# Kernel optimization log

Measured on AMD Instinct MI355X. Metric: run time of the kernel, lower is better.

## Reference

```python
import jax, jax.numpy as jnp
import numpy as np

BETA = 0.25

def setup_inputs() -> dict:
    key = jax.random.key(0)
    k1, k2 = jax.random.split(key)
    N, K, D = 262144, 256, 256
    z_e = jax.random.normal(k1, (N, D), dtype=jnp.float32)
    # nn.Embedding init: uniform(-1/K, 1/K)
    emb_weight = jax.random.uniform(k2, (K, D), dtype=jnp.float32, minval=-1.0 / K, maxval=1.0 / K)
    return {"z_e": z_e, "emb_weight": emb_weight}

def reference(z_e, emb_weight):
    # squared L2 distances: ||z||^2 + ||e||^2 - 2 z e^T  -> [N, K]
    dist = (jnp.sum(z_e ** 2, axis=1, keepdims=True)
            + jnp.sum(emb_weight ** 2, axis=1)
            - 2.0 * jnp.matmul(z_e, emb_weight.T))
    encoding_inds = jnp.argmin(dist, axis=1)  # [N]
    z_q = emb_weight[encoding_inds]           # [N, D]

    sg = jax.lax.stop_gradient
    commitment_loss = jnp.mean((sg(z_e) - z_q) ** 2)
    codebook_loss = jnp.mean((z_e - sg(z_q)) ** 2)
    loss = codebook_loss + BETA * commitment_loss

    # straight-through estimator
    z_q_st = z_e + sg(z_q - z_e)
    return z_q_st, encoding_inds, loss
```

## Files before the change

kernel.cpp:

```cpp
#include <hip/hip_runtime.h>

typedef __attribute__((ext_vector_type(8))) short bf16x8;
typedef __attribute__((ext_vector_type(4))) float f32x4;
typedef __attribute__((ext_vector_type(4))) unsigned short us4;
typedef __attribute__((ext_vector_type(8))) unsigned short us8;

#define NROWS 262144
#define KC 256
#define DD 256
#define BM 64
#define DK 32
#define SW 40
#define TAU 1.5e-3f
#define FCAP 65536

__device__ __forceinline__ float np_pw128_sq(const float* a) {
    float r[8];
#pragma unroll
    for (int j = 0; j < 8; ++j) r[j] = __fmul_rn(a[j], a[j]);
    for (int i = 8; i < 128; i += 8) {
#pragma unroll
        for (int j = 0; j < 8; ++j)
            r[j] = __fadd_rn(r[j], __fmul_rn(a[i + j], a[i + j]));
    }
    float t01 = __fadd_rn(r[0], r[1]), t23 = __fadd_rn(r[2], r[3]);
    float t45 = __fadd_rn(r[4], r[5]), t67 = __fadd_rn(r[6], r[7]);
    return __fadd_rn(__fadd_rn(t01, t23), __fadd_rn(t45, t67));
}
__device__ __forceinline__ float np_sum256_sq(const float* a) {
    return __fadd_rn(np_pw128_sq(a), np_pw128_sq(a + 128));
}

__device__ __forceinline__ unsigned short bf16_rne(float x) {
    unsigned b = __float_as_uint(x);
    b += 0x7FFFu + ((b >> 16) & 1u);
    return (unsigned short)(b >> 16);
}

__global__ void vq_prep(const float* __restrict__ emb, float* __restrict__ se,
                        double* __restrict__ accum, int* __restrict__ gcnt) {
    int k = threadIdx.x;
    if (k == 0) { *accum = 0.0; *gcnt = 0; }
    se[k] = np_sum256_sq(emb + (size_t)k * DD);
}

__global__ void vq_split(const float* __restrict__ emb, unsigned short* __restrict__ ph) {
    int f = (blockIdx.x * 256 + threadIdx.x) * 4;
    float4 v = *reinterpret_cast<const float4*>(emb + f);
    int k = f >> 8, d = f & 255;
    int off = (d >> 5) * (KC * DK) + k * DK + (d & 31);
    us4 h;
    h[0] = bf16_rne(v.x); h[1] = bf16_rne(v.y);
    h[2] = bf16_rne(v.z); h[3] = bf16_rne(v.w);
    *reinterpret_cast<us4*>(ph + off) = h;
}

__global__ __launch_bounds__(256, 3)
void vq_main(const float* __restrict__ ze, const float* __restrict__ emb,
             const unsigned short* __restrict__ ph,
             const float* __restrict__ se_g, float* __restrict__ out_zq,
             float* __restrict__ out_inds, double* __restrict__ accum,
             int* __restrict__ glist, int* __restrict__ gcnt)
{
    __shared__ __attribute__((aligned(16))) unsigned short es[2][KC * SW];
    __shared__ float  se_s[KC];
    __shared__ int    inds_s[BM];
    __shared__ float  red[256];

    const int t = threadIdx.x;
    const int w = t >> 6;
    const int l = t & 63;
    const int q = (t >> 4) & 3;
    const int c = t & 15;
    const size_t m0 = (size_t)blockIdx.x * BM;

    se_s[t] = se_g[t];

    us8 ereg[4];
#pragma unroll
    for (int it = 0; it < 4; ++it)
        ereg[it] = *reinterpret_cast<const us8*>(ph + (it * 256 + t) * 8);

    const float* zrow = ze + (m0 + 16 * w + c) * DD + q * 8;
    float sz_acc = 0.f;
    bf16x8 afrag[8];
#pragma unroll
    for (int pp = 0; pp < 8; pp += 2) {
        float4 a0 = *reinterpret_cast<const float4*>(zrow + pp * 32);
        float4 b0 = *reinterpret_cast<const float4*>(zrow + pp * 32 + 4);
        float4 a1 = *reinterpret_cast<const float4*>(zrow + pp * 32 + 32);
        float4 b1 = *reinterpret_cast<const float4*>(zrow + pp * 32 + 36);
        sz_acc = fmaf(a0.x, a0.x, sz_acc); sz_acc = fmaf(a0.y, a0.y, sz_acc);
        sz_acc = fmaf(a0.z, a0.z, sz_acc); sz_acc = fmaf(a0.w, a0.w, sz_acc);
        sz_acc = fmaf(b0.x, b0.x, sz_acc); sz_acc = fmaf(b0.y, b0.y, sz_acc);
        sz_acc = fmaf(b0.z, b0.z, sz_acc); sz_acc = fmaf(b0.w, b0.w, sz_acc);
        sz_acc = fmaf(a1.x, a1.x, sz_acc); sz_acc = fmaf(a1.y, a1.y, sz_acc);
        sz_acc = fmaf(a1.z, a1.z, sz_acc); sz_acc = fmaf(a1.w, a1.w, sz_acc);
        sz_acc = fmaf(b1.x, b1.x, sz_acc); sz_acc = fmaf(b1.y, b1.y, sz_acc);
        sz_acc = fmaf(b1.z, b1.z, sz_acc); sz_acc = fmaf(b1.w, b1.w, sz_acc);
        us8 h0, h1;
        h0[0] = bf16_rne(a0.x); h0[1] = bf16_rne(a0.y); h0[2] = bf16_rne(a0.z); h0[3] = bf16_rne(a0.w);
        h0[4] = bf16_rne(b0.x); h0[5] = bf16_rne(b0.y); h0[6] = bf16_rne(b0.z); h0[7] = bf16_rne(b0.w);
        h1[0] = bf16_rne(a1.x); h1[1] = bf16_rne(a1.y); h1[2] = bf16_rne(a1.z); h1[3] = bf16_rne(a1.w);
        h1[4] = bf16_rne(b1.x); h1[5] = bf16_rne(b1.y); h1[6] = bf16_rne(b1.z); h1[7] = bf16_rne(b1.w);
        afrag[pp]     = __builtin_bit_cast(bf16x8, h0);
        afrag[pp + 1] = __builtin_bit_cast(bf16x8, h1);
    }

#pragma unroll
    for (int it = 0; it < 4; ++it) {
        int idx = it * 256 + t;
        *reinterpret_cast<us8*>(&es[0][(idx >> 2) * SW + (idx & 3) * 8]) = ereg[it];
    }

    f32x4 acc[16];
#pragma unroll
    for (int i = 0; i < 16; ++i) acc[i] = (f32x4){0.f, 0.f, 0.f, 0.f};

#pragma unroll
    for (int dci = 0; dci < 8; ++dci) {
        __syncthreads();
        if (dci < 7) {
            const unsigned short* ehp = ph + (dci + 1) * (KC * DK);
#pragma unroll
            for (int it = 0; it < 4; ++it)
                ereg[it] = *reinterpret_cast<const us8*>(ehp + (it * 256 + t) * 8);
        }
#pragma unroll
        for (int nf = 0; nf < 16; ++nf) {
            bf16x8 b = *reinterpret_cast<const bf16x8*>(&es[dci & 1][(16 * nf + c) * SW + q * 8]);
            acc[nf] = __builtin_amdgcn_mfma_f32_16x16x32_bf16(afrag[dci], b, acc[nf], 0, 0, 0);
        }
        if (dci < 7) {
#pragma unroll
            for (int it = 0; it < 4; ++it) {
                int idx = it * 256 + t;
                *reinterpret_cast<us8*>(&es[(dci + 1) & 1][(idx >> 2) * SW + (idx & 3) * 8]) = ereg[it];
            }
        }
    }

    float lossv = 0.f;
#pragma unroll
    for (int j = 0; j < 4; ++j) {
        float v1 = 3.4e38f, v2 = 3.4e38f; int k1 = 0x7fffffff;
#pragma unroll
        for (int nf = 0; nf < 16; ++nf) {
            int k = 16 * nf + c;
            float dv = fmaf(-2.f, acc[nf][j], se_s[k]);
            if (dv < v1) { v2 = v1; v1 = dv; k1 = k; }
            else if (dv < v2) { v2 = dv; }
        }
#pragma unroll
        for (int off = 1; off < 16; off <<= 1) {
            float ov1 = __shfl_xor(v1, off, 64);
            float ov2 = __shfl_xor(v2, off, 64);
            int   ok1 = __shfl_xor(k1, off, 64);
            bool other = (ov1 < v1) || (ov1 == v1 && ok1 < k1);
            float nv2 = other ? fminf(v1, ov2) : fminf(v2, ov1);
            if (other) { v1 = ov1; k1 = ok1; }
            v2 = nv2;
        }
        if (c == 0) {
            int row = 16 * w + 4 * q + j;
            inds_s[row] = k1;
            lossv += v1;
            if (v2 - v1 < TAU) {
                int s = atomicAdd(gcnt, 1);
                if (s < FCAP) glist[s] = (int)(m0 + row);
            }
        }
    }
    __syncthreads();

    if (t < BM) out_inds[m0 + t] = (float)inds_s[t];

#pragma unroll
    for (int r = 0; r < 16; ++r) {
        int k = inds_s[16 * w + r];
        float4 v = *reinterpret_cast<const float4*>(emb + (size_t)k * DD + l * 4);
        *reinterpret_cast<float4*>(out_zq + (m0 + 16 * w + r) * DD + l * 4) = v;
    }

    red[t] = sz_acc + lossv;
    __syncthreads();
    for (int s = 128; s > 0; s >>= 1) {
        if (t < s) red[t] += red[t + s];
        __syncthreads();
    }
    if (t == 0) atomicAdd(accum, (double)red[0]);
}

__global__ __launch_bounds__(256)
void vq_fix(const float* __restrict__ ze, const float* __restrict__ emb,
            const float* __restrict__ se_g, const int* __restrict__ glist,
            const int* __restrict__ gcnt, float* __restrict__ out_zq,
            float* __restrict__ out_inds)
{
    __shared__ float dq[16][256];
    __shared__ float srow_s[16];
    __shared__ int   rowid_s[16];
    __shared__ int   klds[16];

    const int t = threadIdx.x;
    int F = *gcnt; if (F > FCAP) F = FCAP;
    const float se_k = se_g[t];
    const float4* e4p = reinterpret_cast<const float4*>(emb + (size_t)t * DD);

    for (int g = blockIdx.x * 16; g < F; g += gridDim.x * 16) {
        __syncthreads();
        if (t < 16) {
            int idx = g + t; if (idx > F - 1) idx = F - 1;
            int row = glist[idx];
            rowid_s[t] = row;
            srow_s[t] = np_sum256_sq(ze + (size_t)row * DD);
        }
        __syncthreads();

        const float* zp[16];
#pragma unroll
        for (int r = 0; r < 16; ++r)
            zp[r] = ze + (size_t)__builtin_amdgcn_readfirstlane(rowid_s[r]) * DD;

        float m32[16];
#pragma unroll
        for (int r = 0; r < 16; ++r) m32[r] = 0.f;
        for (int d4 = 0; d4 < 64; ++d4) {
            float4 e4 = e4p[d4];
            const int d = d4 * 4;
#pragma unroll
            for (int r = 0; r < 16; ++r) {
                m32[r] = __fmaf_rn(zp[r][d + 0], e4.x, m32[r]);
                m32[r] = __fmaf_rn(zp[r][d + 1], e4.y, m32[r]);
                m32[r] = __fmaf_rn(zp[r][d + 2], e4.z, m32[r]);
                m32[r] = __fmaf_rn(zp[r][d + 3], e4.w, m32[r]);
            }
        }
#pragma unroll
        for (int r = 0; r < 16; ++r) {
            float A = __fadd_rn(srow_s[r], se_k);
            dq[r][t] = __fsub_rn(A, __fmul_rn(2.0f, m32[r]));
        }
        __syncthreads();

        {
            const int r = t >> 4, p = t & 15;
            float bv = 3.4e38f; int bk = 0x7fffffff;
#pragma unroll
            for (int i = 0; i < 16; ++i) {
                int k = p * 16 + i;
                float v = dq[r][k];
                if (v < bv) { bv = v; bk = k; }
            }
#pragma unroll
            for (int off = 1; off < 16; off <<= 1) {
                float ov = __shfl_xor(bv, off, 64);
                int   ok = __shfl_xor(bk, off, 64);
                if (ov < bv || (ov == bv && ok < bk)) { bv = ov; bk = ok; }
            }
            if (p == 0) klds[r] = bk;
        }
        __syncthreads();

        int R = F - g; if (R > 16) R = 16;
#pragma unroll
        for (int r = 0; r < 16; ++r) {
            if (r < R) {
                int row = rowid_s[r];
                int kk  = klds[r];
                out_zq[(size_t)row * DD + t] = emb[(size_t)kk * DD + t];
                if (t == 0) out_inds[row] = (float)kk;
            }
        }
    }
}

__global__ void vq_fin(const double* __restrict__ accum, float* __restrict__ out_loss) {
    *out_loss = (float)(1.25 * (*accum) / ((double)NROWS * (double)DD));
}

extern "C" void kernel_launch(void* const* d_in, const int* in_sizes, int n_in,
                              void* d_out, int out_size, void* d_ws, size_t ws_size,
                              hipStream_t stream) {
    const float* ze  = (const float*)d_in[0];
    const float* emb = (const float*)d_in[1];
    float* out      = (float*)d_out;
    float* out_zq   = out;
    float* out_inds = out + (size_t)NROWS * DD;
    float* out_loss = out + (size_t)NROWS * DD + NROWS;

    double* accum = (double*)d_ws;
    int*    gcnt  = (int*)((char*)d_ws + 8);
    float*  se    = (float*)((char*)d_ws + 256);
    int*    glist = (int*)((char*)d_ws + 4096);
    unsigned short* ph = (unsigned short*)((char*)d_ws + 4096 + 262144);

    vq_prep<<<1, 256, 0, stream>>>(emb, se, accum, gcnt);
    vq_split<<<KC * DD / (256 * 4), 256, 0, stream>>>(emb, ph);
    vq_main<<<NROWS / BM, 256, 0, stream>>>(ze, emb, ph, se, out_zq, out_inds,
                                            accum, glist, gcnt);
    vq_fix<<<1024, 256, 0, stream>>>(ze, emb, se, glist, gcnt, out_zq, out_inds);
    vq_fin<<<1, 1, 0, stream>>>(accum, out_loss);
}
```

Measured before the change: 365.4 us.

## Double rows per block and read codebook fragments directly from global memory

The row tile grows from 64 to 128, so each wave computes two 16-row MFMA tiles that share every loaded codebook fragment. The shared-memory double-buffered staging of the bf16 codebook is removed along with its per-chunk barriers, and B fragments are now loaded straight from global memory, relying on L1/L2 caching of the small codebook. This drops LDS traffic and synchronisation and halves the number of blocks. In exchange it doubles accumulator registers, lowers the occupancy target to 2 blocks per CU, and makes every wave fetch the whole codebook through the cache hierarchy.

```diff
diff --git a/kernel.cpp b/kernel.cpp
--- a/kernel.cpp
+++ b/kernel.cpp
@@ -8,9 +8,8 @@
 #define NROWS 262144
 #define KC 256
 #define DD 256
-#define BM 64
+#define BM 128
 #define DK 32
-#define SW 40
 #define TAU 1.5e-3f
 #define FCAP 65536
 
@@ -55,17 +54,16 @@
     *reinterpret_cast<us4*>(ph + off) = h;
 }
 
-__global__ __launch_bounds__(256, 3)
+__global__ __launch_bounds__(256, 2)
 void vq_main(const float* __restrict__ ze, const float* __restrict__ emb,
              const unsigned short* __restrict__ ph,
              const float* __restrict__ se_g, float* __restrict__ out_zq,
              float* __restrict__ out_inds, double* __restrict__ accum,
              int* __restrict__ glist, int* __restrict__ gcnt)
 {
-    __shared__ __attribute__((aligned(16))) unsigned short es[2][KC * SW];
-    __shared__ float  se_s[KC];
-    __shared__ int    inds_s[BM];
-    __shared__ float  red[256];
+    __shared__ float se_s[KC];
+    __shared__ int   inds_s[BM];
+    __shared__ float red[256];
 
     const int t = threadIdx.x;
     const int w = t >> 6;
@@ -75,21 +73,18 @@
     const size_t m0 = (size_t)blockIdx.x * BM;
 
     se_s[t] = se_g[t];
-
-    us8 ereg[4];
-#pragma unroll
-    for (int it = 0; it < 4; ++it)
-        ereg[it] = *reinterpret_cast<const us8*>(ph + (it * 256 + t) * 8);
-
-    const float* zrow = ze + (m0 + 16 * w + c) * DD + q * 8;
+    __syncthreads();
+
+    const float* zr0 = ze + (m0 + 32 * w + c) * DD + q * 8;
+    const float* zr1 = ze + (m0 + 32 * w + 16 + c) * DD + q * 8;
     float sz_acc = 0.f;
-    bf16x8 afrag[8];
-#pragma unroll
-    for (int pp = 0; pp < 8; pp += 2) {
-        float4 a0 = *reinterpret_cast<const float4*>(zrow + pp * 32);
-        float4 b0 = *reinterpret_cast<const float4*>(zrow + pp * 32 + 4);
-        float4 a1 = *reinterpret_cast<const float4*>(zrow + pp * 32 + 32);
-        float4 b1 = *reinterpret_cast<const float4*>(zrow + pp * 32 + 36);
+    bf16x8 af0[8], af1[8];
+#pragma unroll
+    for (int dci = 0; dci < 8; ++dci) {
+        float4 a0 = *reinterpret_cast<const float4*>(zr0 + dci * 32);
+        float4 b0 = *reinterpret_cast<const float4*>(zr0 + dci * 32 + 4);
+        float4 a1 = *reinterpret_cast<const float4*>(zr1 + dci * 32);
+        float4 b1 = *reinterpret_cast<const float4*>(zr1 + dci * 32 + 4);
         sz_acc = fmaf(a0.x, a0.x, sz_acc); sz_acc = fmaf(a0.y, a0.y, sz_acc);
         sz_acc = fmaf(a0.z, a0.z, sz_acc); sz_acc = fmaf(a0.w, a0.w, sz_acc);
         sz_acc = fmaf(b0.x, b0.x, sz_acc); sz_acc = fmaf(b0.y, b0.y, sz_acc);
@@ -103,83 +98,74 @@
         h0[4] = bf16_rne(b0.x); h0[5] = bf16_rne(b0.y); h0[6] = bf16_rne(b0.z); h0[7] = bf16_rne(b0.w);
         h1[0] = bf16_rne(a1.x); h1[1] = bf16_rne(a1.y); h1[2] = bf16_rne(a1.z); h1[3] = bf16_rne(a1.w);
         h1[4] = bf16_rne(b1.x); h1[5] = bf16_rne(b1.y); h1[6] = bf16_rne(b1.z); h1[7] = bf16_rne(b1.w);
-        afrag[pp]     = __builtin_bit_cast(bf16x8, h0);
-        afrag[pp + 1] = __builtin_bit_cast(bf16x8, h1);
-    }
-
-#pragma unroll
-    for (int it = 0; it < 4; ++it) {
-        int idx = it * 256 + t;
-        *reinterpret_cast<us8*>(&es[0][(idx >> 2) * SW + (idx & 3) * 8]) = ereg[it];
-    }
-
-    f32x4 acc[16];
-#pragma unroll
-    for (int i = 0; i < 16; ++i) acc[i] = (f32x4){0.f, 0.f, 0.f, 0.f};
+        af0[dci] = __builtin_bit_cast(bf16x8, h0);
+        af1[dci] = __builtin_bit_cast(bf16x8, h1);
+    }
+
+    f32x4 acc0[16], acc1[16];
+#pragma unroll
+    for (int i = 0; i < 16; ++i) {
+        acc0[i] = (f32x4){0.f, 0.f, 0.f, 0.f};
+        acc1[i] = (f32x4){0.f, 0.f, 0.f, 0.f};
+    }
 
 #pragma unroll
     for (int dci = 0; dci < 8; ++dci) {
-        __syncthreads();
-        if (dci < 7) {
-            const unsigned short* ehp = ph + (dci + 1) * (KC * DK);
-#pragma unroll
-            for (int it = 0; it < 4; ++it)
-                ereg[it] = *reinterpret_cast<const us8*>(ehp + (it * 256 + t) * 8);
-        }
+        const unsigned short* ep = ph + dci * (KC * DK) + c * DK + q * 8;
 #pragma unroll
         for (int nf = 0; nf < 16; ++nf) {
-            bf16x8 b = *reinterpret_cast<const bf16x8*>(&es[dci & 1][(16 * nf + c) * SW + q * 8]);
-            acc[nf] = __builtin_amdgcn_mfma_f32_16x16x32_bf16(afrag[dci], b, acc[nf], 0, 0, 0);
-        }
-        if (dci < 7) {
-#pragma unroll
-            for (int it = 0; it < 4; ++it) {
-                int idx = it * 256 + t;
-                *reinterpret_cast<us8*>(&es[(dci + 1) & 1][(idx >> 2) * SW + (idx & 3) * 8]) = ereg[it];
-            }
+            bf16x8 b = *reinterpret_cast<const bf16x8*>(ep + nf * 16 * DK);
+            acc0[nf] = __builtin_amdgcn_mfma_f32_16x16x32_bf16(af0[dci], b, acc0[nf], 0, 0, 0);
+            acc1[nf] = __builtin_amdgcn_mfma_f32_16x16x32_bf16(af1[dci], b, acc1[nf], 0, 0, 0);
         }
     }
 
     float lossv = 0.f;
-#pragma unroll
-    for (int j = 0; j < 4; ++j) {
-        float v1 = 3.4e38f, v2 = 3.4e38f; int k1 = 0x7fffffff;
-#pragma unroll
-        for (int nf = 0; nf < 16; ++nf) {
-            int k = 16 * nf + c;
-            float dv = fmaf(-2.f, acc[nf][j], se_s[k]);
-            if (dv < v1) { v2 = v1; v1 = dv; k1 = k; }
-            else if (dv < v2) { v2 = dv; }
-        }
-#pragma unroll
-        for (int off = 1; off < 16; off <<= 1) {
-            float ov1 = __shfl_xor(v1, off, 64);
-            float ov2 = __shfl_xor(v2, off, 64);
-            int   ok1 = __shfl_xor(k1, off, 64);
-            bool other = (ov1 < v1) || (ov1 == v1 && ok1 < k1);
-            float nv2 = other ? fminf(v1, ov2) : fminf(v2, ov1);
-            if (other) { v1 = ov1; k1 = ok1; }
-            v2 = nv2;
-        }
-        if (c == 0) {
-            int row = 16 * w + 4 * q + j;
-            inds_s[row] = k1;
-            lossv += v1;
-            if (v2 - v1 < TAU) {
-                int s = atomicAdd(gcnt, 1);
-                if (s < FCAP) glist[s] = (int)(m0 + row);
-            }
-        }
-    }
+#define ARGMIN_SET(ACC, S)                                                     \
+    {                                                                          \
+        _Pragma("unroll")                                                      \
+        for (int j = 0; j < 4; ++j) {                                          \
+            float v1 = 3.4e38f, v2 = 3.4e38f; int k1 = 0x7fffffff;             \
+            _Pragma("unroll")                                                  \
+            for (int nf = 0; nf < 16; ++nf) {                                  \
+                int k = 16 * nf + c;                                           \
+                float dv = fmaf(-2.f, ACC[nf][j], se_s[k]);                    \
+                if (dv < v1) { v2 = v1; v1 = dv; k1 = k; }                     \
+                else if (dv < v2) { v2 = dv; }                                 \
+            }                                                                  \
+            _Pragma("unroll")                                                  \
+            for (int off = 1; off < 16; off <<= 1) {                           \
+                float ov1 = __shfl_xor(v1, off, 64);                           \
+                float ov2 = __shfl_xor(v2, off, 64);                           \
+                int   ok1 = __shfl_xor(k1, off, 64);                           \
+                bool other = (ov1 < v1) || (ov1 == v1 && ok1 < k1);            \
+                float nv2 = other ? fminf(v1, ov2) : fminf(v2, ov1);           \
+                if (other) { v1 = ov1; k1 = ok1; }                             \
+                v2 = nv2;                                                      \
+            }                                                                  \
+            if (c == 0) {                                                      \
+                int row = 32 * w + 16 * (S) + 4 * q + j;                       \
+                inds_s[row] = k1;                                              \
+                lossv += v1;                                                   \
+                if (v2 - v1 < TAU) {                                           \
+                    int s_ = atomicAdd(gcnt, 1);                               \
+                    if (s_ < FCAP) glist[s_] = (int)(m0 + row);                \
+                }                                                              \
+            }                                                                  \
+        }                                                                      \
+    }
+    ARGMIN_SET(acc0, 0)
+    ARGMIN_SET(acc1, 1)
+#undef ARGMIN_SET
     __syncthreads();
 
     if (t < BM) out_inds[m0 + t] = (float)inds_s[t];
 
-#pragma unroll
-    for (int r = 0; r < 16; ++r) {
-        int k = inds_s[16 * w + r];
+#pragma unroll 4
+    for (int r = 0; r < 32; ++r) {
+        int k = inds_s[32 * w + r];
         float4 v = *reinterpret_cast<const float4*>(emb + (size_t)k * DD + l * 4);
-        *reinterpret_cast<float4*>(out_zq + (m0 + 16 * w + r) * DD + l * 4) = v;
+        *reinterpret_cast<float4*>(out_zq + (m0 + 32 * w + r) * DD + l * 4) = v;
     }
 
     red[t] = sz_acc + lossv;
```

Result: slower. 528.5 us (+44.6%).

## Keep whole bf16 codebook resident in LDS with 1024-thread persistent blocks

Applied to the files above, without the earlier changes.

The main kernel now loads the entire bf16 codebook (128 KB) into dynamic shared memory once per block and uses 1024-thread blocks. Each wave loops over four 16-row groups. This replaces the per-64-row double-buffered streaming of codebook chunks from global memory and the per-chunk barriers. The codebook layout is re-swizzled to a 16x32 tile format, and the block reduction now uses wave shuffles. The trade-off is one block per CU with heavy LDS use and lower occupancy, and the B-fragment reads from LDS may hit bank conflicts without padding.

```diff
diff --git a/kernel.cpp b/kernel.cpp
--- a/kernel.cpp
+++ b/kernel.cpp
@@ -8,9 +8,6 @@
 #define NROWS 262144
 #define KC 256
 #define DD 256
-#define BM 64
-#define DK 32
-#define SW 40
 #define TAU 1.5e-3f
 #define FCAP 65536
 
@@ -30,7 +27,6 @@
 __device__ __forceinline__ float np_sum256_sq(const float* a) {
     return __fadd_rn(np_pw128_sq(a), np_pw128_sq(a + 128));
 }
-
 __device__ __forceinline__ unsigned short bf16_rne(float x) {
     unsigned b = __float_as_uint(x);
     b += 0x7FFFu + ((b >> 16) & 1u);
@@ -48,147 +44,144 @@
     int f = (blockIdx.x * 256 + threadIdx.x) * 4;
     float4 v = *reinterpret_cast<const float4*>(emb + f);
     int k = f >> 8, d = f & 255;
-    int off = (d >> 5) * (KC * DK) + k * DK + (d & 31);
+    int off = (d >> 5) * 8192 + (k >> 4) * 512 + (k & 15) * 32 + ((d >> 3) & 3) * 8 + (d & 7);
     us4 h;
     h[0] = bf16_rne(v.x); h[1] = bf16_rne(v.y);
     h[2] = bf16_rne(v.z); h[3] = bf16_rne(v.w);
     *reinterpret_cast<us4*>(ph + off) = h;
 }
 
-__global__ __launch_bounds__(256, 3)
+__global__ __launch_bounds__(1024)
 void vq_main(const float* __restrict__ ze, const float* __restrict__ emb,
-             const unsigned short* __restrict__ ph,
-             const float* __restrict__ se_g, float* __restrict__ out_zq,
-             float* __restrict__ out_inds, double* __restrict__ accum,
-             int* __restrict__ glist, int* __restrict__ gcnt)
+             const unsigned short* __restrict__ ph, const float* __restrict__ se_g,
+             float* __restrict__ out_zq, float* __restrict__ out_inds,
+             double* __restrict__ accum, int* __restrict__ glist, int* __restrict__ gcnt)
 {
-    __shared__ __attribute__((aligned(16))) unsigned short es[2][KC * SW];
-    __shared__ float  se_s[KC];
-    __shared__ int    inds_s[BM];
-    __shared__ float  red[256];
+    extern __shared__ __attribute__((aligned(16))) unsigned short ldsE[];
+    __shared__ float se_s[KC];
+    __shared__ float lred[16];
 
     const int t = threadIdx.x;
-    const int w = t >> 6;
-    const int l = t & 63;
-    const int q = (t >> 4) & 3;
-    const int c = t & 15;
-    const size_t m0 = (size_t)blockIdx.x * BM;
-
-    se_s[t] = se_g[t];
-
-    us8 ereg[4];
-#pragma unroll
-    for (int it = 0; it < 4; ++it)
-        ereg[it] = *reinterpret_cast<const us8*>(ph + (it * 256 + t) * 8);
-
-    const float* zrow = ze + (m0 + 16 * w + c) * DD + q * 8;
-    float sz_acc = 0.f;
-    bf16x8 afrag[8];
-#pragma unroll
-    for (int pp = 0; pp < 8; pp += 2) {
-        float4 a0 = *reinterpret_cast<const float4*>(zrow + pp * 32);
-        float4 b0 = *reinterpret_cast<const float4*>(zrow + pp * 32 + 4);
-        float4 a1 = *reinterpret_cast<const float4*>(zrow + pp * 32 + 32);
-        float4 b1 = *reinterpret_cast<const float4*>(zrow + pp * 32 + 36);
-        sz_acc = fmaf(a0.x, a0.x, sz_acc); sz_acc = fmaf(a0.y, a0.y, sz_acc);
-        sz_acc = fmaf(a0.z, a0.z, sz_acc); sz_acc = fmaf(a0.w, a0.w, sz_acc);
-        sz_acc = fmaf(b0.x, b0.x, sz_acc); sz_acc = fmaf(b0.y, b0.y, sz_acc);
-        sz_acc = fmaf(b0.z, b0.z, sz_acc); sz_acc = fmaf(b0.w, b0.w, sz_acc);
-        sz_acc = fmaf(a1.x, a1.x, sz_acc); sz_acc = fmaf(a1.y, a1.y, sz_acc);
-        sz_acc = fmaf(a1.z, a1.z, sz_acc); sz_acc = fmaf(a1.w, a1.w, sz_acc);
-        sz_acc = fmaf(b1.x, b1.x, sz_acc); sz_acc = fmaf(b1.y, b1.y, sz_acc);
-        sz_acc = fmaf(b1.z, b1.z, sz_acc); sz_acc = fmaf(b1.w, b1.w, sz_acc);
-        us8 h0, h1;
-        h0[0] = bf16_rne(a0.x); h0[1] = bf16_rne(a0.y); h0[2] = bf16_rne(a0.z); h0[3] = bf16_rne(a0.w);
-        h0[4] = bf16_rne(b0.x); h0[5] = bf16_rne(b0.y); h0[6] = bf16_rne(b0.z); h0[7] = bf16_rne(b0.w);
-        h1[0] = bf16_rne(a1.x); h1[1] = bf16_rne(a1.y); h1[2] = bf16_rne(a1.z); h1[3] = bf16_rne(a1.w);
-        h1[4] = bf16_rne(b1.x); h1[5] = bf16_rne(b1.y); h1[6] = bf16_rne(b1.z); h1[7] = bf16_rne(b1.w);
-        afrag[pp]     = __builtin_bit_cast(bf16x8, h0);
-        afrag[pp + 1] = __builtin_bit_cast(bf16x8, h1);
-    }
-
-#pragma unroll
-    for (int it = 0; it < 4; ++it) {
-        int idx = it * 256 + t;
-        *reinterpret_cast<us8*>(&es[0][(idx >> 2) * SW + (idx & 3) * 8]) = ereg[it];
-    }
-
-    f32x4 acc[16];
-#pragma unroll
-    for (int i = 0; i < 16; ++i) acc[i] = (f32x4){0.f, 0.f, 0.f, 0.f};
-
-#pragma unroll
-    for (int dci = 0; dci < 8; ++dci) {
-        __syncthreads();
-        if (dci < 7) {
-            const unsigned short* ehp = ph + (dci + 1) * (KC * DK);
-#pragma unroll
-            for (int it = 0; it < 4; ++it)
-                ereg[it] = *reinterpret_cast<const us8*>(ehp + (it * 256 + t) * 8);
-        }
-#pragma unroll
-        for (int nf = 0; nf < 16; ++nf) {
-            bf16x8 b = *reinterpret_cast<const bf16x8*>(&es[dci & 1][(16 * nf + c) * SW + q * 8]);
-            acc[nf] = __builtin_amdgcn_mfma_f32_16x16x32_bf16(afrag[dci], b, acc[nf], 0, 0, 0);
-        }
-        if (dci < 7) {
-#pragma unroll
-            for (int it = 0; it < 4; ++it) {
-                int idx = it * 256 + t;
-                *reinterpret_cast<us8*>(&es[(dci + 1) & 1][(idx >> 2) * SW + (idx & 3) * 8]) = ereg[it];
-            }
-        }
-    }
-
-    float lossv = 0.f;
-#pragma unroll
-    for (int j = 0; j < 4; ++j) {
-        float v1 = 3.4e38f, v2 = 3.4e38f; int k1 = 0x7fffffff;
-#pragma unroll
-        for (int nf = 0; nf < 16; ++nf) {
-            int k = 16 * nf + c;
-            float dv = fmaf(-2.f, acc[nf][j], se_s[k]);
-            if (dv < v1) { v2 = v1; v1 = dv; k1 = k; }
-            else if (dv < v2) { v2 = dv; }
-        }
-#pragma unroll
-        for (int off = 1; off < 16; off <<= 1) {
-            float ov1 = __shfl_xor(v1, off, 64);
-            float ov2 = __shfl_xor(v2, off, 64);
-            int   ok1 = __shfl_xor(k1, off, 64);
-            bool other = (ov1 < v1) || (ov1 == v1 && ok1 < k1);
-            float nv2 = other ? fminf(v1, ov2) : fminf(v2, ov1);
-            if (other) { v1 = ov1; k1 = ok1; }
-            v2 = nv2;
-        }
-        if (c == 0) {
-            int row = 16 * w + 4 * q + j;
-            inds_s[row] = k1;
-            lossv += v1;
-            if (v2 - v1 < TAU) {
-                int s = atomicAdd(gcnt, 1);
-                if (s < FCAP) glist[s] = (int)(m0 + row);
-            }
-        }
+    const int wv = t >> 6;
+    const int lane = t & 63;
+    const int q = (lane >> 4) & 3;
+    const int c = lane & 15;
+
+    if (t < KC) se_s[t] = se_g[t];
+#pragma unroll
+    for (int i = 0; i < 8; ++i) {
+        int idx = i * 1024 + t;
+        *reinterpret_cast<us8*>(&ldsE[idx * 8]) = *reinterpret_cast<const us8*>(ph + idx * 8);
     }
     __syncthreads();
 
-    if (t < BM) out_inds[m0 + t] = (float)inds_s[t];
-
-#pragma unroll
-    for (int r = 0; r < 16; ++r) {
-        int k = inds_s[16 * w + r];
-        float4 v = *reinterpret_cast<const float4*>(emb + (size_t)k * DD + l * 4);
-        *reinterpret_cast<float4*>(out_zq + (m0 + 16 * w + r) * DD + l * 4) = v;
-    }
-
-    red[t] = sz_acc + lossv;
+    float sz_acc = 0.f, lossv = 0.f;
+
+    for (int s = 0; s < 4; ++s) {
+        const int g = blockIdx.x * 64 + wv * 4 + s;
+        const size_t r0 = (size_t)g * 16;
+
+        bf16x8 zfrag[8];
+        const float* zb = ze + (r0 + c) * DD + q * 8;
+#pragma unroll
+        for (int dp = 0; dp < 4; ++dp) {
+            float4 a0 = *reinterpret_cast<const float4*>(zb + (2 * dp) * 32);
+            float4 b0 = *reinterpret_cast<const float4*>(zb + (2 * dp) * 32 + 4);
+            float4 a1 = *reinterpret_cast<const float4*>(zb + (2 * dp + 1) * 32);
+            float4 b1 = *reinterpret_cast<const float4*>(zb + (2 * dp + 1) * 32 + 4);
+            sz_acc = fmaf(a0.x, a0.x, sz_acc); sz_acc = fmaf(a0.y, a0.y, sz_acc);
+            sz_acc = fmaf(a0.z, a0.z, sz_acc); sz_acc = fmaf(a0.w, a0.w, sz_acc);
+            sz_acc = fmaf(b0.x, b0.x, sz_acc); sz_acc = fmaf(b0.y, b0.y, sz_acc);
+            sz_acc = fmaf(b0.z, b0.z, sz_acc); sz_acc = fmaf(b0.w, b0.w, sz_acc);
+            sz_acc = fmaf(a1.x, a1.x, sz_acc); sz_acc = fmaf(a1.y, a1.y, sz_acc);
+            sz_acc = fmaf(a1.z, a1.z, sz_acc); sz_acc = fmaf(a1.w, a1.w, sz_acc);
+            sz_acc = fmaf(b1.x, b1.x, sz_acc); sz_acc = fmaf(b1.y, b1.y, sz_acc);
+            sz_acc = fmaf(b1.z, b1.z, sz_acc); sz_acc = fmaf(b1.w, b1.w, sz_acc);
+            us8 h0, h1;
+            h0[0] = bf16_rne(a0.x); h0[1] = bf16_rne(a0.y); h0[2] = bf16_rne(a0.z); h0[3] = bf16_rne(a0.w);
+            h0[4] = bf16_rne(b0.x); h0[5] = bf16_rne(b0.y); h0[6] = bf16_rne(b0.z); h0[7] = bf16_rne(b0.w);
+            h1[0] = bf16_rne(a1.x); h1[1] = bf16_rne(a1.y); h1[2] = bf16_rne(a1.z); h1[3] = bf16_rne(a1.w);
+            h1[4] = bf16_rne(b1.x); h1[5] = bf16_rne(b1.y); h1[6] = bf16_rne(b1.z); h1[7] = bf16_rne(b1.w);
+            zfrag[2 * dp]     = __builtin_bit_cast(bf16x8, h0);
+            zfrag[2 * dp + 1] = __builtin_bit_cast(bf16x8, h1);
+        }
+
+        float v1[4], v2[4]; int k1[4];
+#pragma unroll
+        for (int j = 0; j < 4; ++j) { v1[j] = 3.4e38f; v2[j] = 3.4e38f; k1[j] = 0x7fffffff; }
+#pragma unroll
+        for (int p = 0; p < 2; ++p) {
+            f32x4 acc[8];
+#pragma unroll
+            for (int n = 0; n < 8; ++n) acc[n] = (f32x4){0.f, 0.f, 0.f, 0.f};
+#pragma unroll
+            for (int dci = 0; dci < 8; ++dci) {
+#pragma unroll
+                for (int n = 0; n < 8; ++n) {
+                    bf16x8 bf = *reinterpret_cast<const bf16x8*>(
+                        &ldsE[dci * 8192 + (p * 8 + n) * 512 + c * 32 + q * 8]);
+                    acc[n] = __builtin_amdgcn_mfma_f32_16x16x32_bf16(zfrag[dci], bf, acc[n], 0, 0, 0);
+                }
+            }
+#pragma unroll
+            for (int n = 0; n < 8; ++n) {
+                int k = (p * 8 + n) * 16 + c;
+                float sev = se_s[k];
+#pragma unroll
+                for (int j = 0; j < 4; ++j) {
+                    float dv = fmaf(-2.f, acc[n][j], sev);
+                    if (dv < v1[j]) { v2[j] = v1[j]; v1[j] = dv; k1[j] = k; }
+                    else if (dv < v2[j]) { v2[j] = dv; }
+                }
+            }
+        }
+
+#pragma unroll
+        for (int j = 0; j < 4; ++j) {
+#pragma unroll
+            for (int off = 1; off < 16; off <<= 1) {
+                float ov1 = __shfl_xor(v1[j], off, 64);
+                float ov2 = __shfl_xor(v2[j], off, 64);
+                int   ok1 = __shfl_xor(k1[j], off, 64);
+                bool other = (ov1 < v1[j]) || (ov1 == v1[j] && ok1 < k1[j]);
+                float nv2 = other ? fminf(v1[j], ov2) : fminf(v2[j], ov1);
+                if (other) { v1[j] = ov1; k1[j] = ok1; }
+                v2[j] = nv2;
+            }
+            if (c == 0) {
+                size_t row = r0 + 4 * q + j;
+                out_inds[row] = (float)k1[j];
+                lossv += v1[j];
+                if (v2[j] - v1[j] < TAU) {
+                    int s_ = atomicAdd(gcnt, 1);
+                    if (s_ < FCAP) glist[s_] = (int)row;
+                }
+            }
+        }
+
+#pragma unroll
+        for (int j = 0; j < 4; ++j) {
+            size_t row = r0 + 4 * q + j;
+            const float* ep = emb + (size_t)k1[j] * DD;
+            float* op = out_zq + row * DD;
+#pragma unroll
+            for (int i = 0; i < 4; ++i) {
+                float4 v = *reinterpret_cast<const float4*>(ep + (i * 16 + c) * 4);
+                *reinterpret_cast<float4*>(op + (i * 16 + c) * 4) = v;
+            }
+        }
+    }
+
+    float part = sz_acc + lossv;
+#pragma unroll
+    for (int off = 1; off < 64; off <<= 1) part += __shfl_xor(part, off, 64);
+    if (lane == 0) lred[wv] = part;
     __syncthreads();
-    for (int s = 128; s > 0; s >>= 1) {
-        if (t < s) red[t] += red[t + s];
-        __syncthreads();
-    }
-    if (t == 0) atomicAdd(accum, (double)red[0]);
+    if (t == 0) {
+        float s = 0.f;
+        for (int i = 0; i < 16; ++i) s += lred[i];
+        atomicAdd(accum, (double)s);
+    }
 }
 
 __global__ __launch_bounds__(256)
@@ -295,10 +288,13 @@
     int*    glist = (int*)((char*)d_ws + 4096);
     unsigned short* ph = (unsigned short*)((char*)d_ws + 4096 + 262144);
 
+    (void)hipFuncSetAttribute((const void*)vq_main,
+                              hipFuncAttributeMaxDynamicSharedMemorySize, 131072);
+
     vq_prep<<<1, 256, 0, stream>>>(emb, se, accum, gcnt);
     vq_split<<<KC * DD / (256 * 4), 256, 0, stream>>>(emb, ph);
-    vq_main<<<NROWS / BM, 256, 0, stream>>>(ze, emb, ph, se, out_zq, out_inds,
-                                            accum, glist, gcnt);
+    vq_main<<<NROWS / 1024, 1024, 131072, stream>>>(ze, emb, ph, se, out_zq, out_inds,
+                                                    accum, glist, gcnt);
     vq_fix<<<1024, 256, 0, stream>>>(ze, emb, se, glist, gcnt, out_zq, out_inds);
     vq_fin<<<1, 1, 0, stream>>>(accum, out_loss);
 }
```

Result: slower. 1.038 ms (+184.0%).
